# Kernel tuning notes

Hardware: AMD Instinct MI355X
Metric: run time of the kernel (lower is better)

The kernel has to match this reference:

```python
import jax, jax.numpy as jnp
import numpy as np

V = 4
H, W, Z = 32, 64, 13
C = 256
NH = 8
WS = (4, 4, 1)
SS = (2, 2, 0)
HID = 1024


def _layernorm(x, g, b):
    mu = jnp.mean(x, axis=-1, keepdims=True)
    var = jnp.mean((x - mu) ** 2, axis=-1, keepdims=True)
    return (x - mu) * jax.lax.rsqrt(var + 1e-5) * g + b


def setup_inputs() -> dict:
    key = jax.random.key(0)
    ks = jax.random.split(key, 12)
    B = 2
    s = 0.02
    return {
        "x_z": jax.random.normal(ks[0], (B, H, W, Z, C), jnp.float32),
        "x_q": jax.random.normal(ks[1], (B, H, W, Z, C), jnp.float32),
        "x_t": jax.random.normal(ks[2], (B, H, W, Z, C), jnp.float32),
        "x_u": jax.random.normal(ks[3], (B, H, W, Z, C), jnp.float32),
        "qkv_w": jax.random.normal(ks[4], (V, C, 3 * C), jnp.float32) * s,
        "qkv_b": jnp.zeros((V, 3 * C), jnp.float32),
        "proj_w": jax.random.normal(ks[5], (V, C, C), jnp.float32) * s,
        "proj_b": jnp.zeros((V, C), jnp.float32),
        "n1_g": jnp.ones((V, C), jnp.float32),
        "n1_b": jnp.zeros((V, C), jnp.float32),
        "n2_g": jnp.ones((V, C), jnp.float32),
        "n2_b": jnp.zeros((V, C), jnp.float32),
        "fc1_w": jax.random.normal(ks[6], (V, C, HID), jnp.float32) * s,
        "fc1_b": jnp.zeros((V, HID), jnp.float32),
        "fc2_w": jax.random.normal(ks[7], (V, HID, C), jnp.float32) * s,
        "fc2_b": jnp.zeros((V, C), jnp.float32),
    }


def reference(x_z, x_q, x_t, x_u, qkv_w, qkv_b, proj_w, proj_b,
              n1_g, n1_b, n2_g, n2_b, fc1_w, fc1_b, fc2_w, fc2_b):
    x = jnp.stack([x_z, x_q, x_t, x_u], axis=0)  # [V,B,H,W,Z,C]
    B = x.shape[1]
    L = H * W * Z
    w0, w1, w2 = WS
    N = w0 * w1 * w2
    hd = C // NH
    scale = hd ** -0.5

    shortcut = x.reshape(V, B, L, C)
    xn = _layernorm(shortcut, n1_g[:, None, None, :], n1_b[:, None, None, :])
    xs = xn.reshape(V, B, H, W, Z, C)
    # cyclic shift (same sign used for both rolls in the source)
    xs = jnp.roll(xs, shift=SS, axis=(2, 3, 4))
    # window partition -> [V, B_, N, C]
    xw = xs.reshape(V, B, H // w0, w0, W // w1, w1, Z // w2, w2, C)
    xw = xw.transpose(0, 1, 2, 4, 6, 3, 5, 7, 8).reshape(V, -1, N, C)
    B_ = xw.shape[1]

    qkv = jnp.einsum('vbnc,vcd->vbnd', xw, qkv_w) + qkv_b[:, None, None, :]
    qkv = qkv.reshape(V, B_, N, 3, NH, hd).transpose(3, 1, 0, 4, 2, 5)  # [3,B_,V,NH,N,hd]
    q, k, v = qkv[0], qkv[1], qkv[2]
    # per-(variable, head) attention: heads of different variables are concatenated
    attn = jax.nn.softmax(jnp.einsum('bvhnd,bvhmd->bvhnm', q * scale, k), axis=-1)
    ctx = jnp.einsum('bvhnm,bvhmd->bvhnd', attn, v)  # [B_,V,NH,N,hd]
    # faithful to torch reshape (B_, N, V*NH, hd) -> (B_, V*N, C): rows interleave (n, v)
    big = ctx.transpose(0, 3, 1, 2, 4).reshape(B_, V * N, C)
    y = big.reshape(B_, V, N, C).transpose(1, 0, 2, 3)  # slice [:, i*N:(i+1)*N]
    y = jnp.einsum('vbnc,vcd->vbnd', y, proj_w) + proj_b[:, None, None, :]
    # window reverse
    y = y.reshape(V, B, H // w0, W // w1, Z // w2, w0, w1, w2, C)
    y = y.transpose(0, 1, 2, 5, 3, 6, 4, 7, 8).reshape(V, B, H, W, Z, C)
    y = jnp.roll(y, shift=SS, axis=(2, 3, 4))  # same-sign roll (preserves source behavior)
    y = y.reshape(V, B, L, C)

    x2 = shortcut + y
    xm = _layernorm(x2, n2_g[:, None, None, :], n2_b[:, None, None, :])
    h = jax.nn.gelu(jnp.einsum('vblc,vcd->vbld', xm, fc1_w) + fc1_b[:, None, None, :],
                    approximate=False)
    m = jnp.einsum('vbld,vdc->vblc', h, fc2_w) + fc2_b[:, None, None, :]
    out = (x2 + m).reshape(V, B, H, W, Z, C)
    return out  # stacked per-variable outputs in variable_order
```

## Files before the change

kernel.cpp:

```cpp
#include <hip/hip_runtime.h>
#include <hip/hip_bf16.h>
#include <cstdint>
#include <cstddef>

#define DI __device__ __forceinline__

typedef __bf16 bf16_t;
typedef bf16_t bf16x8 __attribute__((ext_vector_type(8)));
typedef float f32x4 __attribute__((ext_vector_type(4)));

constexpr int Vn = 4, Bn = 2, Hn = 32, Wn = 64, Zn = 13, Cn = 256, HIDn = 1024;
constexpr int Ln = Hn * Wn * Zn;
constexpr int BWn = Bn * (Hn / 4) * (Wn / 4) * Zn;
constexpr int PB = Bn * Ln;
constexpr int ROWS = Vn * PB;

DI void gload_lds16(const void* g, void* l) {
  __builtin_amdgcn_global_load_lds(
      (const __attribute__((address_space(1))) void*)g,
      (__attribute__((address_space(3))) void*)l, 16, 0, 0);
}

DI unsigned short f2bf_bits(float f) {
  __hip_bfloat16 h = __float2bfloat16(f);
  return *reinterpret_cast<unsigned short*>(&h);
}

DI float gelu_f(float x) {
  float u = x * x;
  float w = x * fmaf(0.044715f, u, 1.0f);
  float e = __expf(-1.5957691216057308f * w);
  return x * __builtin_amdgcn_rcpf(1.0f + e);
}

__global__ __launch_bounds__(256) void transpose_tile_kernel(
    const float* __restrict__ src, __hip_bfloat16* __restrict__ dst, int K, int N) {
  __shared__ float S[64][65];
  const int n0 = blockIdx.x * 64, k0 = blockIdx.y * 64, v = blockIdx.z;
  const int tc = threadIdx.x & 63, tr = threadIdx.x >> 6;
#pragma unroll
  for (int i = 0; i < 16; ++i) {
    int kk = tr + i * 4;
    S[kk][tc] = src[((size_t)v * K + k0 + kk) * N + n0 + tc];
  }
  __syncthreads();
#pragma unroll
  for (int i = 0; i < 16; ++i) {
    int nn = tr + i * 4;
    dst[((size_t)v * N + n0 + nn) * K + k0 + tc] = __float2bfloat16(S[tc][nn]);
  }
}

__global__ __launch_bounds__(256) void ln1_kernel(
    const float* __restrict__ x0, const float* __restrict__ x1,
    const float* __restrict__ x2i, const float* __restrict__ x3,
    const float* __restrict__ g_, const float* __restrict__ b_,
    __hip_bfloat16* __restrict__ xw) {
  int gw = blockIdx.x * 4 + (threadIdx.x >> 6);
  int lane = threadIdx.x & 63;
  int v = gw / PB;
  int rem = gw - v * PB;
  int bw = rem >> 4, nn = rem & 15;
  int zb = bw % 13;
  int t = bw / 13;
  int wb = t & 15, t2 = t >> 4;
  int hb = t2 & 7, b = t2 >> 3;
  int hs = (hb * 4 + (nn >> 2) + 30) & 31;
  int wsrc = (wb * 4 + (nn & 3) + 62) & 63;
  size_t l = (size_t)(hs * 64 + wsrc) * 13 + zb;
  const float* xv = (v == 0) ? x0 : (v == 1) ? x1 : (v == 2) ? x2i : x3;
  const float* xp = xv + ((size_t)b * Ln + l) * 256;
  float4 val = *(const float4*)(xp + lane * 4);
  float s = val.x + val.y + val.z + val.w;
  float sq = val.x * val.x + val.y * val.y + val.z * val.z + val.w * val.w;
#pragma unroll
  for (int o = 32; o; o >>= 1) {
    s += __shfl_xor(s, o);
    sq += __shfl_xor(sq, o);
  }
  float mean = s * (1.0f / 256.0f);
  float var = sq * (1.0f / 256.0f) - mean * mean;
  float rstd = rsqrtf(var + 1e-5f);
  const float* gg = g_ + v * 256 + lane * 4;
  const float* bb = b_ + v * 256 + lane * 4;
  ushort4 o4;
  o4.x = f2bf_bits((val.x - mean) * rstd * gg[0] + bb[0]);
  o4.y = f2bf_bits((val.y - mean) * rstd * gg[1] + bb[1]);
  o4.z = f2bf_bits((val.z - mean) * rstd * gg[2] + bb[2]);
  o4.w = f2bf_bits((val.w - mean) * rstd * gg[3] + bb[3]);
  *reinterpret_cast<ushort4*>(xw + (size_t)gw * 256 + lane * 4) = o4;
}

__global__ __launch_bounds__(256) void attn_kernel(
    const __hip_bfloat16* __restrict__ qkvp, __hip_bfloat16* __restrict__ ctx) {
  __shared__ float P[4][16][17];
  int b_ = blockIdx.x;
  int v = blockIdx.y;
  int wid = threadIdx.x >> 6, lane = threadIdx.x & 63;
  int lm = lane & 15, hi = lane >> 4;
  const bf16_t* base = (const bf16_t*)qkvp + (size_t)(v * BWn + b_) * 16 * 768;
  const float scale = 0.17677669529663687f;
  f32x4 zero = {0.f, 0.f, 0.f, 0.f};
#pragma unroll
  for (int hh = 0; hh < 2; ++hh) {
    int h = wid + 4 * hh;
    bf16x8 qf = *(const bf16x8*)(base + (size_t)lm * 768 + h * 32 + hi * 8);
    bf16x8 kf = *(const bf16x8*)(base + (size_t)lm * 768 + 256 + h * 32 + hi * 8);
    f32x4 s = __builtin_amdgcn_mfma_f32_16x16x32_bf16(qf, kf, zero, 0, 0, 0);
    float p0[4];
#pragma unroll
    for (int q = 0; q < 4; ++q) {
      float val = s[q] * scale;
      float mx = val;
#pragma unroll
      for (int o = 8; o >= 1; o >>= 1) mx = fmaxf(mx, __shfl_xor(mx, o));
      float e = __expf(val - mx);
      float sum = e;
#pragma unroll
      for (int o = 8; o >= 1; o >>= 1) sum += __shfl_xor(sum, o);
      p0[q] = e * __builtin_amdgcn_rcpf(sum);
    }
#pragma unroll
    for (int q = 0; q < 4; ++q) P[wid][hi * 4 + q][lm] = p0[q];
    bf16x8 pa;
#pragma unroll
    for (int j = 0; j < 8; ++j) pa[j] = (bf16_t)0.f;
    if (hi < 2) {
#pragma unroll
      for (int j = 0; j < 8; ++j) pa[j] = (bf16_t)P[wid][lm][hi * 8 + j];
    }
#pragma unroll
    for (int dh = 0; dh < 2; ++dh) {
      bf16x8 vf;
#pragma unroll
      for (int j = 0; j < 8; ++j) vf[j] = (bf16_t)0.f;
      if (hi < 2) {
#pragma unroll
        for (int j = 0; j < 8; ++j)
          vf[j] = base[(size_t)(hi * 8 + j) * 768 + 512 + h * 32 + dh * 16 + lm];
      }
      f32x4 c = __builtin_amdgcn_mfma_f32_16x16x32_bf16(pa, vf, zero, 0, 0, 0);
#pragma unroll
      for (int q = 0; q < 4; ++q) {
        int n = hi * 4 + q;
        int d = dh * 16 + lm;
        int r = n * 4 + v;
        int vo = r >> 4, no = r & 15;
        ctx[((size_t)(vo * BWn + b_) * 16 + no) * 256 + h * 32 + d] = __float2bfloat16(c[q]);
      }
    }
  }
}

template <int EPI, int K, int N>
__global__ __launch_bounds__(256, 3) void gemm4(
    const __hip_bfloat16* __restrict__ A, const __hip_bfloat16* __restrict__ WT,
    const float* __restrict__ bias, __hip_bfloat16* __restrict__ outb,
    float* __restrict__ outf, const float* __restrict__ xi0,
    const float* __restrict__ xi1, const float* __restrict__ xi2,
    const float* __restrict__ xi3) {
  constexpr int NT = K / 64;
  constexpr int NC = N / 128;
  const int v = blockIdx.z;
  const int x = blockIdx.x;
  const int xcd = x & 7;
  const int j = x >> 3;
  const int c = j % NC;
  const int r = xcd + 8 * (j / NC);
  const int rowBase = r * 128;
  const int colBase = c * 128;

  const bf16_t* Av = (const bf16_t*)A + ((size_t)v * PB + rowBase) * K;
  const bf16_t* Wv = (const bf16_t*)WT + ((size_t)v * N + colBase) * K;

  __shared__ __align__(16) uint8_t smem[40960];
  bf16_t(*As)[64] = (bf16_t(*)[64])smem;
  bf16_t(*Bs)[64] = (bf16_t(*)[64])(smem + 16384);

  const int tid = threadIdx.x, wid = tid >> 6, lane = tid & 63;
  const int wr = wid >> 1, wc = wid & 1;
  const int lm = lane & 15, hi = lane >> 4;
  const int rA = lane >> 3;
  const int lg = (lane & 7) ^ rA;

  f32x4 acc[4][4];
#pragma unroll
  for (int m = 0; m < 4; ++m)
#pragma unroll
    for (int n = 0; n < 4; ++n) acc[m][n] = f32x4{0.f, 0.f, 0.f, 0.f};

  for (int t = 0; t < NT; ++t) {
    if (t) __syncthreads();
#pragma unroll
    for (int g = 0; g < 4; ++g) {
      int grp = wid * 4 + g;
      gload_lds16(Av + (size_t)(grp * 8 + rA) * K + t * 64 + lg * 8, &As[grp * 8][0]);
    }
#pragma unroll
    for (int g = 0; g < 4; ++g) {
      int grp = wid * 4 + g;
      gload_lds16(Wv + (size_t)(grp * 8 + rA) * K + t * 64 + lg * 8, &Bs[grp * 8][0]);
    }
    __syncthreads();
#pragma unroll
    for (int kk = 0; kk < 2; ++kk) {
      bf16x8 af[4], bfv[4];
#pragma unroll
      for (int m = 0; m < 4; ++m) {
        const int rr = wr * 64 + m * 16 + lm;
        af[m] = *(const bf16x8*)&As[rr][((kk * 4 + hi) ^ (lm & 7)) * 8];
      }
#pragma unroll
      for (int n = 0; n < 4; ++n) {
        const int rr = wc * 64 + n * 16 + lm;
        bfv[n] = *(const bf16x8*)&Bs[rr][((kk * 4 + hi) ^ (lm & 7)) * 8];
      }
#pragma unroll
      for (int m = 0; m < 4; ++m)
#pragma unroll
        for (int n = 0; n < 4; ++n)
          acc[m][n] = __builtin_amdgcn_mfma_f32_16x16x32_bf16(af[m], bfv[n], acc[m][n], 0, 0, 0);
    }
  }

  __syncthreads();
  uint8_t* ep = smem + wid * 10240;

  if constexpr (EPI == 0) {
    ushort(*E)[72] = (ushort(*)[72])ep;
    float bcol[4];
#pragma unroll
    for (int n = 0; n < 4; ++n) bcol[n] = bias[v * N + colBase + wc * 64 + n * 16 + lm];
#pragma unroll
    for (int m = 0; m < 4; ++m)
#pragma unroll
      for (int q = 0; q < 4; ++q) {
        int lr = m * 16 + hi * 4 + q;
#pragma unroll
        for (int n = 0; n < 4; ++n) E[lr][n * 16 + lm] = f2bf_bits(acc[m][n][q] + bcol[n]);
      }
    const int pr = lane >> 3, pc = lane & 7;
#pragma unroll
    for (int p = 0; p < 8; ++p) {
      int lr = p * 8 + pr;
      bf16x8 val = *(const bf16x8*)&E[lr][pc * 8];
      size_t grow = (size_t)v * PB + rowBase + wr * 64 + lr;
      int gcol = colBase + wc * 64 + pc * 8;
      *(bf16x8*)&outb[grow * N + gcol] = val;
    }
  } else {
    float(*F)[36] = (float(*)[36])ep;
    const int pr = lane >> 3, pc = lane & 7;
#pragma unroll
    for (int h2 = 0; h2 < 2; ++h2) {
#pragma unroll
      for (int m = 0; m < 4; ++m)
#pragma unroll
        for (int q = 0; q < 4; ++q) {
          int lr = m * 16 + hi * 4 + q;
#pragma unroll
          for (int n2 = 0; n2 < 2; ++n2) F[lr][n2 * 16 + lm] = acc[m][h2 * 2 + n2][q];
        }
#pragma unroll
      for (int p = 0; p < 8; ++p) {
        int lr = p * 8 + pr;
        f32x4 a4 = *(const f32x4*)&F[lr][pc * 4];
        int rowv = rowBase + wr * 64 + lr;
        int gcol = colBase + wc * 64 + h2 * 32 + pc * 4;
        f32x4 b4 = *(const f32x4*)&bias[v * N + gcol];
        int b_ = rowv >> 4, nn = rowv & 15;
        int zb = b_ % 13;
        int tt = b_ / 13;
        int wb = tt & 15, tt2 = tt >> 4;
        int hb = tt2 & 7, bb = tt2 >> 3;
        int h2v = (hb * 4 + (nn >> 2) + 2) & 31;
        int w2v = (wb * 4 + (nn & 3) + 2) & 63;
        size_t l = (size_t)(h2v * 64 + w2v) * 13 + zb;
        const float* xv = (v == 0) ? xi0 : (v == 1) ? xi1 : (v == 2) ? xi2 : xi3;
        f32x4 x4 = *(const f32x4*)(xv + ((size_t)bb * Ln + l) * 256 + gcol);
        f32x4 o4 = a4 + b4 + x4;
        *(f32x4*)(outf + (((size_t)v * Bn + bb) * Ln + l) * 256 + gcol) = o4;
      }
      if (h2 == 0) __builtin_amdgcn_s_waitcnt(0);
    }
  }
}

__global__ __launch_bounds__(512, 4) void mlp_fused5(
    const float* __restrict__ x2,
    const __hip_bfloat16* __restrict__ W1T,
    const __hip_bfloat16* __restrict__ W2T,
    const float* __restrict__ b1, const float* __restrict__ b2,
    const float* __restrict__ g2, const float* __restrict__ bt2,
    float* __restrict__ outp) {
  const int v = blockIdx.z;
  const size_t gRow0 = (size_t)v * PB + (size_t)blockIdx.x * 64;

  __shared__ __align__(16) uint8_t smem[69632];
  uint8_t* hb = smem + 65536;

  const int tid = threadIdx.x, wid = tid >> 6, lane = tid & 63;
  const int lm = lane & 15, hi = lane >> 4;
  const int wa = wid >> 2, wb = wid & 3;
  const int rA = lane >> 3, lg = (lane & 7) ^ rA;

  {
    f32x4 g4 = *(const f32x4*)(g2 + v * 256 + lane * 4);
    f32x4 b4l = *(const f32x4*)(bt2 + v * 256 + lane * 4);
    for (int i = 0; i < 8; ++i) {
      int r = wid * 8 + i;
      const float* xp = x2 + (gRow0 + r) * 256;
      float4 val = *(const float4*)(xp + lane * 4);
      float s = val.x + val.y + val.z + val.w;
      float sq = val.x * val.x + val.y * val.y + val.z * val.z + val.w * val.w;
#pragma unroll
      for (int o = 32; o; o >>= 1) {
        s += __shfl_xor(s, o);
        sq += __shfl_xor(sq, o);
      }
      float mean = s * (1.0f / 256.0f);
      float var = sq * (1.0f / 256.0f) - mean * mean;
      float rstd = rsqrtf(var + 1e-5f);
      ushort4 o4;
      o4.x = f2bf_bits((val.x - mean) * rstd * g4[0] + b4l[0]);
      o4.y = f2bf_bits((val.y - mean) * rstd * g4[1] + b4l[1]);
      o4.z = f2bf_bits((val.z - mean) * rstd * g4[2] + b4l[2]);
      o4.w = f2bf_bits((val.w - mean) * rstd * g4[3] + b4l[3]);
      int gph = ((lm >> 1) ^ (r & 7) ^ hi) & 7;
      *(ushort4*)(smem + hi * 8192 + r * 128 + gph * 16 + (lm & 1) * 8) = o4;
    }
  }
  __syncthreads();

  bf16x8 xnf[4][2];
  {
    int r = wb * 16 + lm;
#pragma unroll
    for (int t = 0; t < 4; ++t)
#pragma unroll
      for (int kk = 0; kk < 2; ++kk) {
        int gph = ((kk * 4 + hi) ^ (r & 7) ^ t) & 7;
        xnf[t][kk] = *(const bf16x8*)(smem + t * 8192 + r * 128 + gph * 16);
      }
  }

  f32x4 acc2[8];
#pragma unroll
  for (int ca = 0; ca < 8; ++ca) acc2[ca] = f32x4{0.f, 0.f, 0.f, 0.f};

  const bf16_t* W1v = (const bf16_t*)W1T + (size_t)v * 1024 * 256;
  const bf16_t* W2v = (const bf16_t*)W2T + (size_t)v * 256 * 1024;

  auto stageW = [&](uint8_t* W1c, uint8_t* W2c, int hc) {
#pragma unroll
    for (int s = 0; s < 2; ++s) {
      int idx = wid * 2 + s;
      int t = idx >> 2, grp = idx & 3;
      gload_lds16(W1v + (size_t)(hc * 32 + grp * 8 + rA) * 256 + t * 64 + lg * 8,
                  W1c + t * 4096 + grp * 1024);
    }
#pragma unroll
    for (int s = 0; s < 2; ++s) {
      int i = wid * 2 + s;
      int p = i * 8 + rA;
      int col = 2 * p + (lg >> 2);
      gload_lds16(W2v + (size_t)col * 1024 + hc * 32 + (lg & 3) * 8, W2c + i * 1024);
    }
  };

  stageW(smem + 32768, smem + 49152, 0);
  __syncthreads();

  for (int hc = 0; hc < 32; ++hc) {
    const int cur = hc & 1;
    uint8_t* W1c = smem + (cur ? 0 : 32768);
    uint8_t* W2c = smem + (cur ? 16384 : 49152);
    if (hc + 1 < 32)
      stageW(smem + (cur ? 32768 : 0), smem + (cur ? 49152 : 16384), hc + 1);

    f32x4 acc1 = f32x4{0.f, 0.f, 0.f, 0.f};
    {
      int hw = wa * 16 + lm;
#pragma unroll
      for (int t = 0; t < 4; ++t)
#pragma unroll
        for (int kk = 0; kk < 2; ++kk) {
          bf16x8 w1f = *(const bf16x8*)(W1c + t * 4096 + hw * 128 +
                                        (((kk * 4 + hi) ^ (hw & 7)) & 7) * 16);
          acc1 = __builtin_amdgcn_mfma_f32_16x16x32_bf16(w1f, xnf[t][kk], acc1, 0, 0, 0);
        }
    }
    {
      f32x4 b1v = *(const f32x4*)&b1[v * 1024 + hc * 32 + wa * 16 + hi * 4];
      ushort4 hp;
      hp.x = f2bf_bits(gelu_f(acc1[0] + b1v[0]));
      hp.y = f2bf_bits(gelu_f(acc1[1] + b1v[1]));
      hp.z = f2bf_bits(gelu_f(acc1[2] + b1v[2]));
      hp.w = f2bf_bits(gelu_f(acc1[3] + b1v[3]));
      int xr = wb * 16 + lm;
      int p = xr >> 1;
      int glog = (xr & 1) * 4 + wa * 2 + (hi >> 1);
      int gph = (glog ^ (p & 7)) & 7;
      *(ushort4*)(hb + p * 128 + gph * 16 + (hi & 1) * 8) = hp;
    }
    __syncthreads();

    {
      int xr = wb * 16 + lm;
      int p = xr >> 1;
      bf16x8 hf = *(const bf16x8*)(hb + p * 128 + ((((xr & 1) * 4 + hi) ^ (p & 7)) & 7) * 16);
#pragma unroll
      for (int ca = 0; ca < 8; ++ca) {
        int col = wa * 128 + ca * 16 + lm;
        int p2 = col >> 1;
        bf16x8 w2f = *(const bf16x8*)(W2c + p2 * 128 +
                                      ((((col & 1) * 4 + hi) ^ (p2 & 7)) & 7) * 16);
        acc2[ca] = __builtin_amdgcn_mfma_f32_16x16x32_bf16(w2f, hf, acc2[ca], 0, 0, 0);
      }
    }
    __syncthreads();
  }

  {
    size_t orow = gRow0 + wb * 16 + lm;
    float* obase = outp + orow * 256;
#pragma unroll
    for (int ca = 0; ca < 8; ++ca) {
      int col = wa * 128 + ca * 16 + hi * 4;
      f32x4 b4 = *(const f32x4*)&b2[v * 256 + col];
      float* o = obase + col;
      f32x4 cur = *(const f32x4*)o;
      f32x4 res = cur + acc2[ca] + b4;
      *(f32x4*)o = res;
    }
  }
}

extern "C" void kernel_launch(void* const* d_in, const int* in_sizes, int n_in,
                              void* d_out, int out_size, void* d_ws, size_t ws_size,
                              hipStream_t stream) {
  const float* x0 = (const float*)d_in[0];
  const float* x1 = (const float*)d_in[1];
  const float* x2i = (const float*)d_in[2];
  const float* x3 = (const float*)d_in[3];
  const float* qkv_w = (const float*)d_in[4];
  const float* qkv_b = (const float*)d_in[5];
  const float* proj_w = (const float*)d_in[6];
  const float* proj_b = (const float*)d_in[7];
  const float* n1g = (const float*)d_in[8];
  const float* n1b = (const float*)d_in[9];
  const float* n2g = (const float*)d_in[10];
  const float* n2b = (const float*)d_in[11];
  const float* fc1_w = (const float*)d_in[12];
  const float* fc1_b = (const float*)d_in[13];
  const float* fc2_w = (const float*)d_in[14];
  const float* fc2_b = (const float*)d_in[15];
  float* out = (float*)d_out;

  uint8_t* ws = (uint8_t*)d_ws;
  size_t off = 0;
  auto alloc = [&](size_t bytes) -> void* {
    void* p = ws + off;
    off += (bytes + 255) & ~(size_t)255;
    return p;
  };
  __hip_bfloat16* wqkvT = (__hip_bfloat16*)alloc((size_t)Vn * Cn * 768 * 2);
  __hip_bfloat16* wprojT = (__hip_bfloat16*)alloc((size_t)Vn * Cn * Cn * 2);
  __hip_bfloat16* wfc1T = (__hip_bfloat16*)alloc((size_t)Vn * Cn * HIDn * 2);
  __hip_bfloat16* wfc2T = (__hip_bfloat16*)alloc((size_t)Vn * HIDn * Cn * 2);
  __hip_bfloat16* xw = (__hip_bfloat16*)alloc((size_t)ROWS * Cn * 2);
  __hip_bfloat16* qkvb = (__hip_bfloat16*)alloc((size_t)ROWS * 768 * 2);

  transpose_tile_kernel<<<dim3(768 / 64, 256 / 64, Vn), 256, 0, stream>>>(qkv_w, wqkvT, 256, 768);
  transpose_tile_kernel<<<dim3(256 / 64, 256 / 64, Vn), 256, 0, stream>>>(proj_w, wprojT, 256, 256);
  transpose_tile_kernel<<<dim3(1024 / 64, 256 / 64, Vn), 256, 0, stream>>>(fc1_w, wfc1T, 256, 1024);
  transpose_tile_kernel<<<dim3(256 / 64, 1024 / 64, Vn), 256, 0, stream>>>(fc2_w, wfc2T, 1024, 256);

  ln1_kernel<<<ROWS / 4, 256, 0, stream>>>(x0, x1, x2i, x3, n1g, n1b, xw);

  gemm4<0, 256, 768><<<dim3(416 * 6, 1, Vn), 256, 0, stream>>>(
      xw, wqkvT, qkv_b, qkvb, nullptr, nullptr, nullptr, nullptr, nullptr);

  attn_kernel<<<dim3(BWn, Vn), 256, 0, stream>>>(qkvb, xw );

  gemm4<1, 256, 256><<<dim3(416 * 2, 1, Vn), 256, 0, stream>>>(
      xw , wprojT, proj_b, nullptr, out , x0, x1, x2i, x3);

  mlp_fused5<<<dim3(PB / 64, 1, Vn), 512, 0, stream>>>(
      out , wfc1T, wfc2T, fc1_b, fc2_b, n2g, n2b, out);
}
```

Measured before the change: 860.4 us.

## Double MLP row tile to 128 rows per block with per-wave full-width outputs

The fused MLP kernel now processes 128 rows per block instead of 64. Each of the 8 waves owns 16 rows and computes all 32 hidden columns and all 256 output columns, instead of splitting the work 2x4 across waves. Each staged FC1/FC2 weight chunk is therefore reused across twice as many rows, which halves total weight traffic and grid size. The cost is doubled accumulator registers (16 f32x4 acc2), a larger LDS footprint that may lower occupancy, and an extra sync before the first staging, since the weight buffer now overlaps the LayerNorm staging area.

```diff
diff --git a/kernel.cpp b/kernel.cpp
--- a/kernel.cpp
+++ b/kernel.cpp
@@ -286,7 +286,7 @@
   }
 }
 
-__global__ __launch_bounds__(512, 4) void mlp_fused5(
+__global__ __launch_bounds__(512, 4) void mlp_fused6(
     const float* __restrict__ x2,
     const __hip_bfloat16* __restrict__ W1T,
     const __hip_bfloat16* __restrict__ W2T,
@@ -294,21 +294,20 @@
     const float* __restrict__ g2, const float* __restrict__ bt2,
     float* __restrict__ outp) {
   const int v = blockIdx.z;
-  const size_t gRow0 = (size_t)v * PB + (size_t)blockIdx.x * 64;
-
-  __shared__ __align__(16) uint8_t smem[69632];
+  const size_t gRow0 = (size_t)v * PB + (size_t)blockIdx.x * 128;
+
+  __shared__ __align__(16) uint8_t smem[73728];
   uint8_t* hb = smem + 65536;
 
   const int tid = threadIdx.x, wid = tid >> 6, lane = tid & 63;
   const int lm = lane & 15, hi = lane >> 4;
-  const int wa = wid >> 2, wb = wid & 3;
   const int rA = lane >> 3, lg = (lane & 7) ^ rA;
 
   {
     f32x4 g4 = *(const f32x4*)(g2 + v * 256 + lane * 4);
     f32x4 b4l = *(const f32x4*)(bt2 + v * 256 + lane * 4);
-    for (int i = 0; i < 8; ++i) {
-      int r = wid * 8 + i;
+    for (int i = 0; i < 16; ++i) {
+      int r = wid * 16 + i;
       const float* xp = x2 + (gRow0 + r) * 256;
       float4 val = *(const float4*)(xp + lane * 4);
       float s = val.x + val.y + val.z + val.w;
@@ -327,26 +326,26 @@
       o4.z = f2bf_bits((val.z - mean) * rstd * g4[2] + b4l[2]);
       o4.w = f2bf_bits((val.w - mean) * rstd * g4[3] + b4l[3]);
       int gph = ((lm >> 1) ^ (r & 7) ^ hi) & 7;
-      *(ushort4*)(smem + hi * 8192 + r * 128 + gph * 16 + (lm & 1) * 8) = o4;
+      *(ushort4*)(smem + hi * 16384 + r * 128 + gph * 16 + (lm & 1) * 8) = o4;
     }
   }
   __syncthreads();
 
   bf16x8 xnf[4][2];
   {
-    int r = wb * 16 + lm;
+    int r = wid * 16 + lm;
 #pragma unroll
     for (int t = 0; t < 4; ++t)
 #pragma unroll
       for (int kk = 0; kk < 2; ++kk) {
         int gph = ((kk * 4 + hi) ^ (r & 7) ^ t) & 7;
-        xnf[t][kk] = *(const bf16x8*)(smem + t * 8192 + r * 128 + gph * 16);
-      }
-  }
-
-  f32x4 acc2[8];
-#pragma unroll
-  for (int ca = 0; ca < 8; ++ca) acc2[ca] = f32x4{0.f, 0.f, 0.f, 0.f};
+        xnf[t][kk] = *(const bf16x8*)(smem + t * 16384 + r * 128 + gph * 16);
+      }
+  }
+
+  f32x4 acc2[16];
+#pragma unroll
+  for (int ca = 0; ca < 16; ++ca) acc2[ca] = f32x4{0.f, 0.f, 0.f, 0.f};
 
   const bf16_t* W1v = (const bf16_t*)W1T + (size_t)v * 1024 * 256;
   const bf16_t* W2v = (const bf16_t*)W2T + (size_t)v * 256 * 1024;
@@ -368,19 +367,23 @@
     }
   };
 
-  stageW(smem + 32768, smem + 49152, 0);
+  __syncthreads();
+  stageW(smem, smem + 16384, 0);
   __syncthreads();
 
   for (int hc = 0; hc < 32; ++hc) {
     const int cur = hc & 1;
-    uint8_t* W1c = smem + (cur ? 0 : 32768);
-    uint8_t* W2c = smem + (cur ? 16384 : 49152);
+    uint8_t* W1c = smem + (cur ? 32768 : 0);
+    uint8_t* W2c = smem + (cur ? 49152 : 16384);
     if (hc + 1 < 32)
-      stageW(smem + (cur ? 32768 : 0), smem + (cur ? 49152 : 16384), hc + 1);
-
-    f32x4 acc1 = f32x4{0.f, 0.f, 0.f, 0.f};
-    {
-      int hw = wa * 16 + lm;
+      stageW(smem + (cur ? 0 : 32768), smem + (cur ? 16384 : 49152), hc + 1);
+
+    int xr = wid * 16 + lm;
+    int p = xr >> 1;
+#pragma unroll
+    for (int t2 = 0; t2 < 2; ++t2) {
+      f32x4 acc1 = f32x4{0.f, 0.f, 0.f, 0.f};
+      int hw = t2 * 16 + lm;
 #pragma unroll
       for (int t = 0; t < 4; ++t)
 #pragma unroll
@@ -389,29 +392,23 @@
                                         (((kk * 4 + hi) ^ (hw & 7)) & 7) * 16);
           acc1 = __builtin_amdgcn_mfma_f32_16x16x32_bf16(w1f, xnf[t][kk], acc1, 0, 0, 0);
         }
-    }
-    {
-      f32x4 b1v = *(const f32x4*)&b1[v * 1024 + hc * 32 + wa * 16 + hi * 4];
+      f32x4 b1v = *(const f32x4*)&b1[v * 1024 + hc * 32 + t2 * 16 + hi * 4];
       ushort4 hp;
       hp.x = f2bf_bits(gelu_f(acc1[0] + b1v[0]));
       hp.y = f2bf_bits(gelu_f(acc1[1] + b1v[1]));
       hp.z = f2bf_bits(gelu_f(acc1[2] + b1v[2]));
       hp.w = f2bf_bits(gelu_f(acc1[3] + b1v[3]));
-      int xr = wb * 16 + lm;
-      int p = xr >> 1;
-      int glog = (xr & 1) * 4 + wa * 2 + (hi >> 1);
+      int glog = (xr & 1) * 4 + t2 * 2 + (hi >> 1);
       int gph = (glog ^ (p & 7)) & 7;
       *(ushort4*)(hb + p * 128 + gph * 16 + (hi & 1) * 8) = hp;
     }
     __syncthreads();
 
     {
-      int xr = wb * 16 + lm;
-      int p = xr >> 1;
       bf16x8 hf = *(const bf16x8*)(hb + p * 128 + ((((xr & 1) * 4 + hi) ^ (p & 7)) & 7) * 16);
 #pragma unroll
-      for (int ca = 0; ca < 8; ++ca) {
-        int col = wa * 128 + ca * 16 + lm;
+      for (int ca = 0; ca < 16; ++ca) {
+        int col = ca * 16 + lm;
         int p2 = col >> 1;
         bf16x8 w2f = *(const bf16x8*)(W2c + p2 * 128 +
                                       ((((col & 1) * 4 + hi) ^ (p2 & 7)) & 7) * 16);
@@ -422,11 +419,11 @@
   }
 
   {
-    size_t orow = gRow0 + wb * 16 + lm;
+    size_t orow = gRow0 + wid * 16 + lm;
     float* obase = outp + orow * 256;
 #pragma unroll
-    for (int ca = 0; ca < 8; ++ca) {
-      int col = wa * 128 + ca * 16 + hi * 4;
+    for (int ca = 0; ca < 16; ++ca) {
+      int col = ca * 16 + hi * 4;
       f32x4 b4 = *(const f32x4*)&b2[v * 256 + col];
       float* o = obase + col;
       f32x4 cur = *(const f32x4*)o;
@@ -486,6 +483,6 @@
   gemm4<1, 256, 256><<<dim3(416 * 2, 1, Vn), 256, 0, stream>>>(
       xw , wprojT, proj_b, nullptr, out , x0, x1, x2i, x3);
 
-  mlp_fused5<<<dim3(PB / 64, 1, Vn), 512, 0, stream>>>(
+  mlp_fused6<<<dim3(PB / 128, 1, Vn), 512, 0, stream>>>(
       out , wfc1T, wfc2T, fc1_b, fc2_b, n2g, n2b, out);
 }
```

After: 908.1 us. 5.5% more time.
